# Kernel tuning notes

Measured on AMD Instinct MI355X. Metric: run time of the kernel, lower is better.

The kernel has to match this reference:

```python
import jax, jax.numpy as jnp
import numpy as np

B, S, D, H = 4, 2048, 768, 12
HD = D // H           # 64, also BigBird block size
BS, NB = 64, S // 64  # block size, num blocks
DFF = 4 * D
NEG = jnp.float32(-1e9)


def _bigbird_block_mask():
    # window(3) + global(first/last block rows+cols) + 3 random blocks per row
    rng = np.random.default_rng(0)
    m = np.zeros((NB, NB), dtype=bool)
    idx = np.arange(NB)
    for off in (-1, 0, 1):
        m[idx, np.clip(idx + off, 0, NB - 1)] = True
    m[0, :] = True; m[-1, :] = True; m[:, 0] = True; m[:, -1] = True
    rand_cols = rng.integers(0, NB, size=(NB, 3))
    m[idx[:, None], rand_cols] = True
    return m


def setup_inputs() -> dict:
    key = jax.random.key(0)
    ks = jax.random.split(key, 12)
    sc = 0.02
    inp = {
        "q": jax.random.normal(ks[0], (B, S, D), jnp.float32),
        "encoder_out": jax.random.normal(ks[1], (B, S, D), jnp.float32),
        "bb_mask": jnp.asarray(_bigbird_block_mask()),
        "Wq_s": jax.random.normal(ks[2], (D, D), jnp.float32) * sc,
        "Wk_s": jax.random.normal(ks[3], (D, D), jnp.float32) * sc,
        "Wv_s": jax.random.normal(ks[4], (D, D), jnp.float32) * sc,
        "Wo_s": jax.random.normal(ks[5], (D, D), jnp.float32) * sc,
        "Wq_c": jax.random.normal(ks[6], (D, D), jnp.float32) * sc,
        "Wk_c": jax.random.normal(ks[7], (D, D), jnp.float32) * sc,
        "Wv_c": jax.random.normal(ks[8], (D, D), jnp.float32) * sc,
        "Wo_c": jax.random.normal(ks[9], (D, D), jnp.float32) * sc,
        "ln_g": jnp.ones((D,), jnp.float32),
        "ln_b": jnp.zeros((D,), jnp.float32),
        "W1": jax.random.normal(ks[10], (D, DFF), jnp.float32) * sc,
        "b1": jnp.zeros((DFF,), jnp.float32),
        "W2": jax.random.normal(ks[11], (DFF, D), jnp.float32) * sc,
        "b2": jnp.zeros((D,), jnp.float32),
    }
    return inp


def _ln(x, g, b):
    mu = jnp.mean(x, -1, keepdims=True)
    var = jnp.mean(jnp.square(x - mu), -1, keepdims=True)
    return (x - mu) * jax.lax.rsqrt(var + 1e-5) * g + b


def _mha(xq, xkv, Wq, Wk, Wv, Wo, mask):
    # mask: [Sq, Sk] bool, True = attend
    b, sq, _ = xq.shape
    sk = xkv.shape[1]
    q = (xq @ Wq).reshape(b, sq, H, HD).transpose(0, 2, 1, 3)
    k = (xkv @ Wk).reshape(b, sk, H, HD).transpose(0, 2, 1, 3)
    v = (xkv @ Wv).reshape(b, sk, H, HD).transpose(0, 2, 1, 3)
    scores = jnp.einsum('bhqd,bhkd->bhqk', q, k) / jnp.sqrt(jnp.float32(HD))
    scores = jnp.where(mask[None, None], scores, NEG)
    attn = jax.nn.softmax(scores, axis=-1)
    o = jnp.einsum('bhqk,bhkd->bhqd', attn, v).transpose(0, 2, 1, 3).reshape(b, sq, D)
    return o @ Wo


def reference(q, encoder_out, bb_mask,
              Wq_s, Wk_s, Wv_s, Wo_s,
              Wq_c, Wk_c, Wv_c, Wo_c,
              ln_g, ln_b, W1, b1, W2, b2):
    # expand block mask to element level [S, S]
    el = jnp.repeat(jnp.repeat(bb_mask, BS, axis=0), BS, axis=1)
    causal = jnp.tril(jnp.ones((S, S), bool))
    m_self = el & causal
    x = q + _mha(_ln(q, ln_g, ln_b), _ln(q, ln_g, ln_b), Wq_s, Wk_s, Wv_s, Wo_s, m_self)
    x = x + _mha(_ln(x, ln_g, ln_b), encoder_out, Wq_c, Wk_c, Wv_c, Wo_c, el)
    h = _ln(x, ln_g, ln_b)
    x = x + (jax.nn.relu(h @ W1 + b1) @ W2 + b2)
    return x
```

## Files before the change

### kernel.cpp

```cpp
#include <hip/hip_runtime.h>
#include <hip/hip_bf16.h>

#define S_LEN 2048
#define DIM   768
#define NHEAD 12
#define HDIM  64
#define NBLK  32
#define BTOK  8192
#define DFF_  3072

typedef __attribute__((ext_vector_type(8))) short bf16x8;
typedef __attribute__((ext_vector_type(4))) float f32x4;

__device__ __forceinline__ void glds16(const void* g, void* l) {
  __builtin_amdgcn_global_load_lds(
      (const __attribute__((address_space(1))) void*)g,
      (__attribute__((address_space(3))) void*)l, 16, 0, 0);
}

__device__ __forceinline__ unsigned short bfbits(float f) {
  __hip_bfloat16 t = __float2bfloat16(f);
  return *(unsigned short*)&t;
}

__global__ void mask_norm_k(const unsigned char* __restrict__ p,
                            unsigned char* __restrict__ out) {
  int i = blockIdx.x * 256 + threadIdx.x;
  if (i < NBLK * NBLK) {
    bool byteLayout = (p[1] != 0);
    out[i] = byteLayout ? (unsigned char)(p[i] != 0)
                        : (unsigned char)(((const int*)p)[i] != 0);
  }
}

__device__ __forceinline__ float blockReduceSum256(float v) {
  v += __shfl_down(v, 32); v += __shfl_down(v, 16); v += __shfl_down(v, 8);
  v += __shfl_down(v, 4);  v += __shfl_down(v, 2);  v += __shfl_down(v, 1);
  __shared__ float sm[4];
  int w = threadIdx.x >> 6;
  __syncthreads();
  if ((threadIdx.x & 63) == 0) sm[w] = v;
  __syncthreads();
  return sm[0] + sm[1] + sm[2] + sm[3];
}

__global__ __launch_bounds__(256) void ln_k(const float* __restrict__ x,
                                            const float* __restrict__ g,
                                            const float* __restrict__ b,
                                            __hip_bfloat16* __restrict__ y) {
  size_t row = blockIdx.x;
  const float* xr = x + row * DIM;
  int t = threadIdx.x;
  float v0 = xr[t], v1 = xr[t + 256], v2 = xr[t + 512];
  float tot = blockReduceSum256(v0 + v1 + v2);
  float mu = tot * (1.0f / DIM);
  float d0 = v0 - mu, d1 = v1 - mu, d2 = v2 - mu;
  float var = blockReduceSum256(d0 * d0 + d1 * d1 + d2 * d2) * (1.0f / DIM);
  float rstd = rsqrtf(var + 1e-5f);
  __hip_bfloat16* yr = y + row * DIM;
  yr[t]       = __float2bfloat16(d0 * rstd * g[t]       + b[t]);
  yr[t + 256] = __float2bfloat16(d1 * rstd * g[t + 256] + b[t + 256]);
  yr[t + 512] = __float2bfloat16(d2 * rstd * g[t + 512] + b[t + 512]);
}

__global__ __launch_bounds__(256) void castbf_k(const float* __restrict__ x,
                                                __hip_bfloat16* __restrict__ y,
                                                int n) {
  int i = (blockIdx.x * 256 + threadIdx.x) * 8;
  if (i < n) {
    float4 v0 = *(const float4*)(x + i);
    float4 v1 = *(const float4*)(x + i + 4);
    union { bf16x8 v; unsigned short u[8]; } pk;
    pk.u[0] = bfbits(v0.x); pk.u[1] = bfbits(v0.y);
    pk.u[2] = bfbits(v0.z); pk.u[3] = bfbits(v0.w);
    pk.u[4] = bfbits(v1.x); pk.u[5] = bfbits(v1.y);
    pk.u[6] = bfbits(v1.z); pk.u[7] = bfbits(v1.w);
    *(bf16x8*)((unsigned short*)y + i) = pk.v;
  }
}

__global__ __launch_bounds__(256) void tcast_k(const float* __restrict__ W,
                                               __hip_bfloat16* __restrict__ Wt,
                                               int R, int C) {
  __shared__ float T[64][65];
  int r0 = blockIdx.y * 64, c0 = blockIdx.x * 64;
  int t = threadIdx.x;
  int r = t >> 2, cg = (t & 3) * 16;
  #pragma unroll
  for (int ii = 0; ii < 16; ii += 4) {
    float4 v = *(const float4*)(W + (size_t)(r0 + r) * C + c0 + cg + ii);
    T[r][cg + ii + 0] = v.x; T[r][cg + ii + 1] = v.y;
    T[r][cg + ii + 2] = v.z; T[r][cg + ii + 3] = v.w;
  }
  __syncthreads();
  int oc = t >> 2, og = (t & 3) * 16;
  union { bf16x8 v; unsigned short u[8]; } p0, p1;
  #pragma unroll
  for (int ii = 0; ii < 8; ++ii) p0.u[ii] = bfbits(T[og + ii][oc]);
  #pragma unroll
  for (int ii = 0; ii < 8; ++ii) p1.u[ii] = bfbits(T[og + 8 + ii][oc]);
  unsigned short* dst = (unsigned short*)Wt + (size_t)(c0 + oc) * R + r0 + og;
  *(bf16x8*)dst = p0.v;
  *(bf16x8*)(dst + 8) = p1.v;
}

template<bool BF16OUT, bool HASBIAS, bool HASRES, bool RELU, bool TRANSV>
__global__ __launch_bounds__(256) void mgemm_k(
    const __hip_bfloat16* __restrict__ A,
    const __hip_bfloat16* __restrict__ Bt,
    const float* __restrict__ bias,
    const float* __restrict__ resid,
    void* __restrict__ Cout,
    int M, int N, int K) {
  __shared__ char Asl[128 * 128];
  __shared__ char Bsl[128 * 128];
  int tid = threadIdx.x, w = tid >> 6, lane = tid & 63;
  int g = lane >> 4, cc = lane & 15;
  int wr = w >> 1, wc = w & 1;
  int m0 = blockIdx.y * 128, n0 = blockIdx.x * 128;

  f32x4 acc[4][4];
  #pragma unroll
  for (int i = 0; i < 4; ++i)
    #pragma unroll
    for (int j = 0; j < 4; ++j) acc[i][j] = (f32x4){0.f, 0.f, 0.f, 0.f};

  for (int k0 = 0; k0 < K; k0 += 64) {
    __syncthreads();
    #pragma unroll
    for (int ii = 0; ii < 4; ++ii) {
      int chunk = ii * 256 + w * 64 + lane;
      int row = chunk >> 3, hh = chunk & 7;
      int koff = k0 + ((hh ^ (row & 7)) << 3);
      glds16(A  + (size_t)(m0 + row) * K + koff, Asl + (ii * 256 + w * 64) * 16);
      glds16(Bt + (size_t)(n0 + row) * K + koff, Bsl + (ii * 256 + w * 64) * 16);
    }
    __syncthreads();
    bf16x8 a[4][2], b[4][2];
    #pragma unroll
    for (int i = 0; i < 4; ++i)
      #pragma unroll
      for (int s = 0; s < 2; ++s) {
        int row = wr * 64 + i * 16 + cc;
        a[i][s] = *(const bf16x8*)(Asl + row * 128 + (((s * 4 + g) ^ (cc & 7)) << 4));
      }
    #pragma unroll
    for (int j = 0; j < 4; ++j)
      #pragma unroll
      for (int s = 0; s < 2; ++s) {
        int row = wc * 64 + j * 16 + cc;
        b[j][s] = *(const bf16x8*)(Bsl + row * 128 + (((s * 4 + g) ^ (cc & 7)) << 4));
      }
    #pragma unroll
    for (int i = 0; i < 4; ++i)
      #pragma unroll
      for (int j = 0; j < 4; ++j)
        #pragma unroll
        for (int s = 0; s < 2; ++s)
          acc[i][j] = __builtin_amdgcn_mfma_f32_16x16x32_bf16(a[i][s], b[j][s], acc[i][j], 0, 0, 0);
  }
  #pragma unroll
  for (int i = 0; i < 4; ++i)
    #pragma unroll
    for (int j = 0; j < 4; ++j)
      #pragma unroll
      for (int e = 0; e < 4; ++e) {
        int r   = m0 + wr * 64 + i * 16 + g * 4 + e;
        int col = n0 + wc * 64 + j * 16 + cc;
        float v = acc[i][j][e];
        if (HASBIAS) v += bias[col];
        if (HASRES)  v += resid[(size_t)r * N + col];
        if (RELU)    v = fmaxf(v, 0.f);
        if (TRANSV) {
          int bb = r >> 11, s = r & 2047;
          ((__hip_bfloat16*)Cout)[(size_t)bb * DIM * S_LEN + (size_t)col * S_LEN + s] = __float2bfloat16(v);
        } else if (BF16OUT) {
          ((__hip_bfloat16*)Cout)[(size_t)r * N + col] = __float2bfloat16(v);
        } else {
          ((float*)Cout)[(size_t)r * N + col] = v;
        }
      }
}

template<bool CAUSAL>
__global__ __launch_bounds__(64) void mattn_k(
    const __hip_bfloat16* __restrict__ Qg,
    const __hip_bfloat16* __restrict__ Kg,
    const __hip_bfloat16* __restrict__ Vtg,
    __hip_bfloat16* __restrict__ O,
    const unsigned char* __restrict__ mask) {
  __shared__ char Ps[2048];
  int strip = blockIdx.x, h = blockIdx.y, b = blockIdx.z;
  int qb = strip >> 2, wq = strip & 3;
  int lane = threadIdx.x;
  int g = lane >> 4, cc = lane & 15;
  const unsigned short* Qp = (const unsigned short*)Qg;
  const unsigned short* Kp = (const unsigned short*)Kg;
  const unsigned short* Vp = (const unsigned short*)Vtg;

  bf16x8 aq[2];
  size_t qrow = ((size_t)b * S_LEN + strip * 16 + cc) * DIM + h * HDIM;
  aq[0] = *(const bf16x8*)(Qp + qrow + g * 8);
  aq[1] = *(const bf16x8*)(Qp + qrow + (4 + g) * 8);

  float m_[4], l_[4];
  f32x4 accO[4];
  #pragma unroll
  for (int e = 0; e < 4; ++e) { m_[e] = -3.0e38f; l_[e] = 0.f; }
  #pragma unroll
  for (int j = 0; j < 4; ++j) accO[j] = (f32x4){0.f, 0.f, 0.f, 0.f};

  int kbEnd = CAUSAL ? (qb + 1) : NBLK;
  for (int kb = 0; kb < kbEnd; ++kb) {
    if (!mask[qb * NBLK + kb]) continue;

    f32x4 S[4];
    #pragma unroll
    for (int j = 0; j < 4; ++j) S[j] = (f32x4){0.f, 0.f, 0.f, 0.f};
    #pragma unroll
    for (int j = 0; j < 4; ++j) {
      size_t krow = ((size_t)b * S_LEN + kb * 64 + j * 16 + cc) * DIM + h * HDIM;
      bf16x8 bk0 = *(const bf16x8*)(Kp + krow + g * 8);
      bf16x8 bk1 = *(const bf16x8*)(Kp + krow + (4 + g) * 8);
      S[j] = __builtin_amdgcn_mfma_f32_16x16x32_bf16(aq[0], bk0, S[j], 0, 0, 0);
      S[j] = __builtin_amdgcn_mfma_f32_16x16x32_bf16(aq[1], bk1, S[j], 0, 0, 0);
    }

    float p_[4][4];
    #pragma unroll
    for (int e = 0; e < 4; ++e) {
      float mm = -3.0e38f;
      #pragma unroll
      for (int j = 0; j < 4; ++j) {
        float sv = S[j][e] * 0.125f;
        if (CAUSAL && kb == qb) {
          int ql = wq * 16 + g * 4 + e, kl = j * 16 + cc;
          if (kl > ql) sv = -1e9f;
        }
        p_[j][e] = sv;
        mm = fmaxf(mm, sv);
      }
      mm = fmaxf(mm, __shfl_xor(mm, 1));
      mm = fmaxf(mm, __shfl_xor(mm, 2));
      mm = fmaxf(mm, __shfl_xor(mm, 4));
      mm = fmaxf(mm, __shfl_xor(mm, 8));
      float newm = fmaxf(m_[e], mm);
      float corr = __expf(m_[e] - newm);
      float rs = 0.f;
      #pragma unroll
      for (int j = 0; j < 4; ++j) {
        float p = __expf(p_[j][e] - newm);
        p_[j][e] = p;
        rs += p;
      }
      rs += __shfl_xor(rs, 1); rs += __shfl_xor(rs, 2);
      rs += __shfl_xor(rs, 4); rs += __shfl_xor(rs, 8);
      l_[e] = l_[e] * corr + rs;
      m_[e] = newm;
      #pragma unroll
      for (int j = 0; j < 4; ++j) accO[j][e] *= corr;
      int ql = g * 4 + e;
      #pragma unroll
      for (int j = 0; j < 4; ++j) {
        int kv = j * 16 + cc;
        int byt = ql * 128 + ((((kv >> 3) ^ (ql & 7))) << 4) + ((kv & 7) << 1);
        *(unsigned short*)(Ps + byt) = bfbits(p_[j][e]);
      }
    }

    #pragma unroll
    for (int s = 0; s < 2; ++s) {
      bf16x8 ap = *(const bf16x8*)(Ps + cc * 128 + (((s * 4 + g) ^ (cc & 7)) << 4));
      #pragma unroll
      for (int j = 0; j < 4; ++j) {
        size_t vrow = ((size_t)b * DIM + h * HDIM + j * 16 + cc) * S_LEN + kb * 64;
        bf16x8 bv = *(const bf16x8*)(Vp + vrow + (s * 4 + g) * 8);
        accO[j] = __builtin_amdgcn_mfma_f32_16x16x32_bf16(ap, bv, accO[j], 0, 0, 0);
      }
    }
  }
  #pragma unroll
  for (int e = 0; e < 4; ++e) {
    float inv = 1.0f / fmaxf(l_[e], 1e-30f);
    int tok = b * S_LEN + strip * 16 + g * 4 + e;
    #pragma unroll
    for (int j = 0; j < 4; ++j)
      O[(size_t)tok * DIM + h * HDIM + j * 16 + cc] = __float2bfloat16(accO[j][e] * inv);
  }
}

extern "C" void kernel_launch(void* const* d_in, const int* in_sizes, int n_in,
                              void* d_out, int out_size, void* d_ws, size_t ws_size,
                              hipStream_t stream) {
  const float* q    = (const float*)d_in[0];
  const float* enc  = (const float*)d_in[1];
  const unsigned char* bbm = (const unsigned char*)d_in[2];
  const float* Wsrc[8] = {(const float*)d_in[3], (const float*)d_in[4],
                          (const float*)d_in[5], (const float*)d_in[6],
                          (const float*)d_in[7], (const float*)d_in[8],
                          (const float*)d_in[9], (const float*)d_in[10]};
  const float* ln_g = (const float*)d_in[11];
  const float* ln_b = (const float*)d_in[12];
  const float* W1   = (const float*)d_in[13];
  const float* b1   = (const float*)d_in[14];
  const float* W2   = (const float*)d_in[15];
  const float* b2   = (const float*)d_in[16];

  char* ws = (char*)d_ws;
  unsigned char* maskn = (unsigned char*)ws;
  const size_t WT1 = (size_t)DIM * DIM * 2;
  __hip_bfloat16* Wt[8];
  for (int i = 0; i < 8; ++i) Wt[i] = (__hip_bfloat16*)(ws + 4096 + i * WT1);
  __hip_bfloat16* W1t  = (__hip_bfloat16*)(ws + 9441280);
  __hip_bfloat16* W2t  = (__hip_bfloat16*)(ws + 14159872);
  __hip_bfloat16* Ebf  = (__hip_bfloat16*)(ws + 18878464);
  float*          X    = (float*)         (ws + 31461376);
  __hip_bfloat16* Abf  = (__hip_bfloat16*)(ws + 56627200);
  __hip_bfloat16* Bq   = (__hip_bfloat16*)(ws + 69210112);
  __hip_bfloat16* Bk   = (__hip_bfloat16*)(ws + 81793024);
  __hip_bfloat16* Vt   = (__hip_bfloat16*)(ws + 94375936);
  __hip_bfloat16* Cc   = (__hip_bfloat16*)(ws + 106958848);
  __hip_bfloat16* F    = Bq;

  dim3 blk(256);
  dim3 gsq(12, 12), gw1(48, 12), gw2(12, 48);
  dim3 g768(6, 64), gff(24, 64);
  dim3 ga(128, NHEAD, 4);
  dim3 wv(64);

  mask_norm_k<<<4, blk, 0, stream>>>(bbm, maskn);
  for (int i = 0; i < 8; ++i)
    tcast_k<<<gsq, blk, 0, stream>>>(Wsrc[i], Wt[i], DIM, DIM);
  tcast_k<<<gw1, blk, 0, stream>>>(W1, W1t, DIM, DFF_);
  tcast_k<<<gw2, blk, 0, stream>>>(W2, W2t, DFF_, DIM);
  castbf_k<<<3072, blk, 0, stream>>>(enc, Ebf, BTOK * DIM);

  ln_k<<<BTOK, blk, 0, stream>>>(q, ln_g, ln_b, Abf);
  mgemm_k<true,false,false,false,false><<<g768, blk, 0, stream>>>(Abf, Wt[0], nullptr, nullptr, Bq, BTOK, DIM, DIM);
  mgemm_k<true,false,false,false,false><<<g768, blk, 0, stream>>>(Abf, Wt[1], nullptr, nullptr, Bk, BTOK, DIM, DIM);
  mgemm_k<true,false,false,false,true ><<<g768, blk, 0, stream>>>(Abf, Wt[2], nullptr, nullptr, Vt, BTOK, DIM, DIM);
  mattn_k<true><<<ga, wv, 0, stream>>>(Bq, Bk, Vt, Cc, maskn);
  mgemm_k<false,false,true,false,false><<<g768, blk, 0, stream>>>(Cc, Wt[3], nullptr, q, X, BTOK, DIM, DIM);

  ln_k<<<BTOK, blk, 0, stream>>>(X, ln_g, ln_b, Abf);
  mgemm_k<true,false,false,false,false><<<g768, blk, 0, stream>>>(Abf, Wt[4], nullptr, nullptr, Bq, BTOK, DIM, DIM);
  mgemm_k<true,false,false,false,false><<<g768, blk, 0, stream>>>(Ebf, Wt[5], nullptr, nullptr, Bk, BTOK, DIM, DIM);
  mgemm_k<true,false,false,false,true ><<<g768, blk, 0, stream>>>(Ebf, Wt[6], nullptr, nullptr, Vt, BTOK, DIM, DIM);
  mattn_k<false><<<ga, wv, 0, stream>>>(Bq, Bk, Vt, Cc, maskn);
  mgemm_k<false,false,true,false,false><<<g768, blk, 0, stream>>>(Cc, Wt[7], nullptr, X, X, BTOK, DIM, DIM);

  ln_k<<<BTOK, blk, 0, stream>>>(X, ln_g, ln_b, Abf);
  mgemm_k<true,true,false,true,false><<<gff, blk, 0, stream>>>(Abf, W1t, b1, nullptr, F, BTOK, DFF_, DIM);
  mgemm_k<false,true,true,false,false><<<g768, blk, 0, stream>>>(F, W2t, b2, X, d_out, BTOK, DIM, DFF_);

  (void)in_sizes; (void)n_in; (void)out_size; (void)ws_size;
}
```

Before: 895.8 us.

## Group four attention waves per block, prefetch next K/V tile, remap grid

The sparse attention kernel now launches 256-thread blocks in which four waves cover the four 16-row strips of one query block, each with its own LDS slice for P. K and V fragments for the next active key block are loaded into registers while the current block is computed, so global load latency overlaps the MFMA and softmax work. The 1D grid is remapped with an 8-way interleave over (batch, head, query-block) slots to spread work across dispatch. This adds register pressure from the double-buffered K/V fragments, which may lower occupancy. The causal kernel also gives blocks uneven work.

```diff
diff --git a/kernel.cpp b/kernel.cpp
--- a/kernel.cpp
+++ b/kernel.cpp
@@ -182,26 +182,47 @@
       }
 }
 
+#define LOADK(kbv, dst)                                                       \
+  { _Pragma("unroll")                                                         \
+    for (int j = 0; j < 4; ++j) {                                             \
+      size_t kro = ((size_t)b * S_LEN + (kbv) * 64 + j * 16 + cc) * DIM       \
+                   + h * HDIM + g * 8;                                        \
+      dst[j][0] = *(const bf16x8*)(Kp + kro);                                 \
+      dst[j][1] = *(const bf16x8*)(Kp + kro + 32);                            \
+    } }
+#define LOADV(kbv, dst)                                                       \
+  { _Pragma("unroll")                                                         \
+    for (int j = 0; j < 4; ++j) {                                             \
+      size_t vro = ((size_t)b * DIM + h * HDIM + j * 16 + cc) * S_LEN         \
+                   + (kbv) * 64 + g * 8;                                      \
+      dst[j][0] = *(const bf16x8*)(Vp + vro);                                 \
+      dst[j][1] = *(const bf16x8*)(Vp + vro + 32);                            \
+    } }
+
 template<bool CAUSAL>
-__global__ __launch_bounds__(64) void mattn_k(
+__global__ __launch_bounds__(256) void mattn_k(
     const __hip_bfloat16* __restrict__ Qg,
     const __hip_bfloat16* __restrict__ Kg,
     const __hip_bfloat16* __restrict__ Vtg,
     __hip_bfloat16* __restrict__ O,
     const unsigned char* __restrict__ mask) {
-  __shared__ char Ps[2048];
-  int strip = blockIdx.x, h = blockIdx.y, b = blockIdx.z;
-  int qb = strip >> 2, wq = strip & 3;
-  int lane = threadIdx.x;
+  __shared__ char Ps[8192];
+  int lin = blockIdx.x;
+  int slot = (lin & 7) * 192 + (lin >> 3);
+  int pair = slot >> 5, qb = slot & 31;
+  int h = pair % NHEAD, b = pair / NHEAD;
+  int t = threadIdx.x, w = t >> 6, lane = t & 63;
   int g = lane >> 4, cc = lane & 15;
+  int strip = qb * 4 + w;
+  char* Pw = Ps + w * 2048;
   const unsigned short* Qp = (const unsigned short*)Qg;
   const unsigned short* Kp = (const unsigned short*)Kg;
   const unsigned short* Vp = (const unsigned short*)Vtg;
 
-  bf16x8 aq[2];
+  bf16x8 aq0, aq1;
   size_t qrow = ((size_t)b * S_LEN + strip * 16 + cc) * DIM + h * HDIM;
-  aq[0] = *(const bf16x8*)(Qp + qrow + g * 8);
-  aq[1] = *(const bf16x8*)(Qp + qrow + (4 + g) * 8);
+  aq0 = *(const bf16x8*)(Qp + qrow + g * 8);
+  aq1 = *(const bf16x8*)(Qp + qrow + (4 + g) * 8);
 
   float m_[4], l_[4];
   f32x4 accO[4];
@@ -210,20 +231,27 @@
   #pragma unroll
   for (int j = 0; j < 4; ++j) accO[j] = (f32x4){0.f, 0.f, 0.f, 0.f};
 
+  const unsigned char* mrow = mask + qb * NBLK;
   int kbEnd = CAUSAL ? (qb + 1) : NBLK;
-  for (int kb = 0; kb < kbEnd; ++kb) {
-    if (!mask[qb * NBLK + kb]) continue;
+
+  int cur = 0;
+  while (!mrow[cur]) ++cur;
+  bf16x8 kc[4][2], vc[4][2];
+  LOADK(cur, kc); LOADV(cur, vc);
+
+  for (;;) {
+    int nxt = cur + 1;
+    while (nxt < kbEnd && !mrow[nxt]) ++nxt;
+    bool more = (nxt < kbEnd);
+    bf16x8 kn[4][2], vn[4][2];
+    if (more) { LOADK(nxt, kn); LOADV(nxt, vn); }
 
     f32x4 S[4];
     #pragma unroll
-    for (int j = 0; j < 4; ++j) S[j] = (f32x4){0.f, 0.f, 0.f, 0.f};
-    #pragma unroll
     for (int j = 0; j < 4; ++j) {
-      size_t krow = ((size_t)b * S_LEN + kb * 64 + j * 16 + cc) * DIM + h * HDIM;
-      bf16x8 bk0 = *(const bf16x8*)(Kp + krow + g * 8);
-      bf16x8 bk1 = *(const bf16x8*)(Kp + krow + (4 + g) * 8);
-      S[j] = __builtin_amdgcn_mfma_f32_16x16x32_bf16(aq[0], bk0, S[j], 0, 0, 0);
-      S[j] = __builtin_amdgcn_mfma_f32_16x16x32_bf16(aq[1], bk1, S[j], 0, 0, 0);
+      S[j] = (f32x4){0.f, 0.f, 0.f, 0.f};
+      S[j] = __builtin_amdgcn_mfma_f32_16x16x32_bf16(aq0, kc[j][0], S[j], 0, 0, 0);
+      S[j] = __builtin_amdgcn_mfma_f32_16x16x32_bf16(aq1, kc[j][1], S[j], 0, 0, 0);
     }
 
     float p_[4][4];
@@ -233,8 +261,8 @@
       #pragma unroll
       for (int j = 0; j < 4; ++j) {
         float sv = S[j][e] * 0.125f;
-        if (CAUSAL && kb == qb) {
-          int ql = wq * 16 + g * 4 + e, kl = j * 16 + cc;
+        if (CAUSAL && cur == qb) {
+          int ql = w * 16 + g * 4 + e, kl = j * 16 + cc;
           if (kl > ql) sv = -1e9f;
         }
         p_[j][e] = sv;
@@ -264,21 +292,27 @@
       for (int j = 0; j < 4; ++j) {
         int kv = j * 16 + cc;
         int byt = ql * 128 + ((((kv >> 3) ^ (ql & 7))) << 4) + ((kv & 7) << 1);
-        *(unsigned short*)(Ps + byt) = bfbits(p_[j][e]);
+        *(unsigned short*)(Pw + byt) = bfbits(p_[j][e]);
       }
     }
 
     #pragma unroll
     for (int s = 0; s < 2; ++s) {
-      bf16x8 ap = *(const bf16x8*)(Ps + cc * 128 + (((s * 4 + g) ^ (cc & 7)) << 4));
-      #pragma unroll
-      for (int j = 0; j < 4; ++j) {
-        size_t vrow = ((size_t)b * DIM + h * HDIM + j * 16 + cc) * S_LEN + kb * 64;
-        bf16x8 bv = *(const bf16x8*)(Vp + vrow + (s * 4 + g) * 8);
-        accO[j] = __builtin_amdgcn_mfma_f32_16x16x32_bf16(ap, bv, accO[j], 0, 0, 0);
-      }
-    }
-  }
+      bf16x8 ap = *(const bf16x8*)(Pw + cc * 128 + (((s * 4 + g) ^ (cc & 7)) << 4));
+      #pragma unroll
+      for (int j = 0; j < 4; ++j)
+        accO[j] = __builtin_amdgcn_mfma_f32_16x16x32_bf16(ap, vc[j][s], accO[j], 0, 0, 0);
+    }
+
+    if (!more) break;
+    #pragma unroll
+    for (int j = 0; j < 4; ++j) {
+      kc[j][0] = kn[j][0]; kc[j][1] = kn[j][1];
+      vc[j][0] = vn[j][0]; vc[j][1] = vn[j][1];
+    }
+    cur = nxt;
+  }
+
   #pragma unroll
   for (int e = 0; e < 4; ++e) {
     float inv = 1.0f / fmaxf(l_[e], 1e-30f);
@@ -325,8 +359,7 @@
   dim3 blk(256);
   dim3 gsq(12, 12), gw1(48, 12), gw2(12, 48);
   dim3 g768(6, 64), gff(24, 64);
-  dim3 ga(128, NHEAD, 4);
-  dim3 wv(64);
+  dim3 ga(1536);
 
   mask_norm_k<<<4, blk, 0, stream>>>(bbm, maskn);
   for (int i = 0; i < 8; ++i)
@@ -339,14 +372,14 @@
   mgemm_k<true,false,false,false,false><<<g768, blk, 0, stream>>>(Abf, Wt[0], nullptr, nullptr, Bq, BTOK, DIM, DIM);
   mgemm_k<true,false,false,false,false><<<g768, blk, 0, stream>>>(Abf, Wt[1], nullptr, nullptr, Bk, BTOK, DIM, DIM);
   mgemm_k<true,false,false,false,true ><<<g768, blk, 0, stream>>>(Abf, Wt[2], nullptr, nullptr, Vt, BTOK, DIM, DIM);
-  mattn_k<true><<<ga, wv, 0, stream>>>(Bq, Bk, Vt, Cc, maskn);
+  mattn_k<true><<<ga, blk, 0, stream>>>(Bq, Bk, Vt, Cc, maskn);
   mgemm_k<false,false,true,false,false><<<g768, blk, 0, stream>>>(Cc, Wt[3], nullptr, q, X, BTOK, DIM, DIM);
 
   ln_k<<<BTOK, blk, 0, stream>>>(X, ln_g, ln_b, Abf);
   mgemm_k<true,false,false,false,false><<<g768, blk, 0, stream>>>(Abf, Wt[4], nullptr, nullptr, Bq, BTOK, DIM, DIM);
   mgemm_k<true,false,false,false,false><<<g768, blk, 0, stream>>>(Ebf, Wt[5], nullptr, nullptr, Bk, BTOK, DIM, DIM);
   mgemm_k<true,false,false,false,true ><<<g768, blk, 0, stream>>>(Ebf, Wt[6], nullptr, nullptr, Vt, BTOK, DIM, DIM);
-  mattn_k<false><<<ga, wv, 0, stream>>>(Bq, Bk, Vt, Cc, maskn);
+  mattn_k<false><<<ga, blk, 0, stream>>>(Bq, Bk, Vt, Cc, maskn);
   mgemm_k<false,false,true,false,false><<<g768, blk, 0, stream>>>(Cc, Wt[7], nullptr, X, X, BTOK, DIM, DIM);
 
   ln_k<<<BTOK, blk, 0, stream>>>(X, ln_g, ln_b, Abf);
```

After: 864.8 us. 1.04x faster.

## Fuse QKV projections and restructure sparse attention with lazy rescaling and balanced scheduling

Applied to the files above, without the earlier changes.

The self-attention Q/K/V projections become one GEMM with N=2304 over the contiguous transposed weights, and the cross-attention K/V projections become one GEMM with N=1536. The epilogue routes each 768-column range to its own buffer, writing V transposed. The attention kernel now computes S transposed (K as the A operand), so softmax needs fewer cross-lane reductions. It prefetches K and V fragments into registers, rescales the running max lazily only when it grows by more than 8, packs P stores into 64-bit writes, and remaps the flat grid so causal-heavy query blocks are spread across XCDs. The aims are fewer launches, fewer re-reads of the A activations, less softmax shuffle and exp overhead, and better load balance. The cost is more register pressure and per-element branching in the GEMM epilogue.

```diff
diff --git a/kernel.cpp b/kernel.cpp
--- a/kernel.cpp
+++ b/kernel.cpp
@@ -18,9 +18,9 @@
       (__attribute__((address_space(3))) void*)l, 16, 0, 0);
 }
 
-__device__ __forceinline__ unsigned short bfbits(float f) {
+__device__ __forceinline__ unsigned int bfbits(float f) {
   __hip_bfloat16 t = __float2bfloat16(f);
-  return *(unsigned short*)&t;
+  return (unsigned int)*(unsigned short*)&t;
 }
 
 __global__ void mask_norm_k(const unsigned char* __restrict__ p,
@@ -104,13 +104,13 @@
   *(bf16x8*)(dst + 8) = p1.v;
 }
 
-template<bool BF16OUT, bool HASBIAS, bool HASRES, bool RELU, bool TRANSV>
+template<bool BF16OUT, bool HASBIAS, bool HASRES, bool RELU, int SPLIT>
 __global__ __launch_bounds__(256) void mgemm_k(
     const __hip_bfloat16* __restrict__ A,
     const __hip_bfloat16* __restrict__ Bt,
     const float* __restrict__ bias,
     const float* __restrict__ resid,
-    void* __restrict__ Cout,
+    void* __restrict__ o1, void* __restrict__ o2, void* __restrict__ o3,
     int M, int N, int K) {
   __shared__ char Asl[128 * 128];
   __shared__ char Bsl[128 * 128];
@@ -159,6 +159,7 @@
         for (int s = 0; s < 2; ++s)
           acc[i][j] = __builtin_amdgcn_mfma_f32_16x16x32_bf16(a[i][s], b[j][s], acc[i][j], 0, 0, 0);
   }
+  int range = n0 / 768;
   #pragma unroll
   for (int i = 0; i < 4; ++i)
     #pragma unroll
@@ -171,13 +172,20 @@
         if (HASBIAS) v += bias[col];
         if (HASRES)  v += resid[(size_t)r * N + col];
         if (RELU)    v = fmaxf(v, 0.f);
-        if (TRANSV) {
-          int bb = r >> 11, s = r & 2047;
-          ((__hip_bfloat16*)Cout)[(size_t)bb * DIM * S_LEN + (size_t)col * S_LEN + s] = __float2bfloat16(v);
-        } else if (BF16OUT) {
-          ((__hip_bfloat16*)Cout)[(size_t)r * N + col] = __float2bfloat16(v);
+        if (SPLIT == 0) {
+          if (BF16OUT) ((__hip_bfloat16*)o1)[(size_t)r * N + col] = __float2bfloat16(v);
+          else         ((float*)o1)[(size_t)r * N + col] = v;
         } else {
-          ((float*)Cout)[(size_t)r * N + col] = v;
+          int cl = col - range * 768;
+          void* dst; bool trans;
+          if (SPLIT == 1) { dst = range == 0 ? o1 : (range == 1 ? o2 : o3); trans = (range == 2); }
+          else            { dst = range == 0 ? o1 : o2;                      trans = (range == 1); }
+          if (trans) {
+            int bb = r >> 11, s = r & 2047;
+            ((__hip_bfloat16*)dst)[(size_t)bb * DIM * S_LEN + (size_t)cl * S_LEN + s] = __float2bfloat16(v);
+          } else {
+            ((__hip_bfloat16*)dst)[(size_t)r * 768 + cl] = __float2bfloat16(v);
+          }
         }
       }
 }
@@ -190,98 +198,123 @@
     __hip_bfloat16* __restrict__ O,
     const unsigned char* __restrict__ mask) {
   __shared__ char Ps[2048];
-  int strip = blockIdx.x, h = blockIdx.y, b = blockIdx.z;
-  int qb = strip >> 2, wq = strip & 3;
+  int lin = blockIdx.x;
+  int slot = (lin & 7) * 768 + (lin >> 3);
+  int pair = slot >> 7, sl = slot & 127;
+  int rawqb = sl >> 2, w = sl & 3;
+  int qb = CAUSAL ? (31 - rawqb)
+                  : ((rawqb & 1) ? (31 - (rawqb >> 1)) : (rawqb >> 1));
+  int h = pair % NHEAD, b = pair / NHEAD;
   int lane = threadIdx.x;
   int g = lane >> 4, cc = lane & 15;
+  int strip = qb * 4 + w;
   const unsigned short* Qp = (const unsigned short*)Qg;
   const unsigned short* Kp = (const unsigned short*)Kg;
   const unsigned short* Vp = (const unsigned short*)Vtg;
 
-  bf16x8 aq[2];
+  bf16x8 aq0, aq1;
   size_t qrow = ((size_t)b * S_LEN + strip * 16 + cc) * DIM + h * HDIM;
-  aq[0] = *(const bf16x8*)(Qp + qrow + g * 8);
-  aq[1] = *(const bf16x8*)(Qp + qrow + (4 + g) * 8);
-
-  float m_[4], l_[4];
+  aq0 = *(const bf16x8*)(Qp + qrow + g * 8);
+  aq1 = *(const bf16x8*)(Qp + qrow + (4 + g) * 8);
+
+  float m_ = -1e30f, l_ = 0.f;
   f32x4 accO[4];
   #pragma unroll
-  for (int e = 0; e < 4; ++e) { m_[e] = -3.0e38f; l_[e] = 0.f; }
-  #pragma unroll
   for (int j = 0; j < 4; ++j) accO[j] = (f32x4){0.f, 0.f, 0.f, 0.f};
 
+  const unsigned char* mrow = mask + qb * NBLK;
   int kbEnd = CAUSAL ? (qb + 1) : NBLK;
+
   for (int kb = 0; kb < kbEnd; ++kb) {
-    if (!mask[qb * NBLK + kb]) continue;
+    if (!mrow[kb]) continue;
+
+    bf16x8 kc[4][2], vc[4][2];
+    #pragma unroll
+    for (int j = 0; j < 4; ++j) {
+      size_t kro = ((size_t)b * S_LEN + kb * 64 + j * 16 + cc) * DIM + h * HDIM + g * 8;
+      kc[j][0] = *(const bf16x8*)(Kp + kro);
+      kc[j][1] = *(const bf16x8*)(Kp + kro + 32);
+      size_t vro = ((size_t)b * DIM + h * HDIM + j * 16 + cc) * S_LEN + kb * 64 + g * 8;
+      vc[j][0] = *(const bf16x8*)(Vp + vro);
+      vc[j][1] = *(const bf16x8*)(Vp + vro + 32);
+    }
 
     f32x4 S[4];
     #pragma unroll
-    for (int j = 0; j < 4; ++j) S[j] = (f32x4){0.f, 0.f, 0.f, 0.f};
-    #pragma unroll
     for (int j = 0; j < 4; ++j) {
-      size_t krow = ((size_t)b * S_LEN + kb * 64 + j * 16 + cc) * DIM + h * HDIM;
-      bf16x8 bk0 = *(const bf16x8*)(Kp + krow + g * 8);
-      bf16x8 bk1 = *(const bf16x8*)(Kp + krow + (4 + g) * 8);
-      S[j] = __builtin_amdgcn_mfma_f32_16x16x32_bf16(aq[0], bk0, S[j], 0, 0, 0);
-      S[j] = __builtin_amdgcn_mfma_f32_16x16x32_bf16(aq[1], bk1, S[j], 0, 0, 0);
-    }
-
-    float p_[4][4];
-    #pragma unroll
-    for (int e = 0; e < 4; ++e) {
-      float mm = -3.0e38f;
-      #pragma unroll
-      for (int j = 0; j < 4; ++j) {
+      S[j] = (f32x4){0.f, 0.f, 0.f, 0.f};
+      S[j] = __builtin_amdgcn_mfma_f32_16x16x32_bf16(kc[j][0], aq0, S[j], 0, 0, 0);
+      S[j] = __builtin_amdgcn_mfma_f32_16x16x32_bf16(kc[j][1], aq1, S[j], 0, 0, 0);
+    }
+
+    float p[4][4];
+    float mmL = -1e30f;
+    #pragma unroll
+    for (int j = 0; j < 4; ++j)
+      #pragma unroll
+      for (int e = 0; e < 4; ++e) {
         float sv = S[j][e] * 0.125f;
         if (CAUSAL && kb == qb) {
-          int ql = wq * 16 + g * 4 + e, kl = j * 16 + cc;
-          if (kl > ql) sv = -1e9f;
+          int kwi = j * 16 + g * 4 + e, qwi = w * 16 + cc;
+          if (kwi > qwi) sv = -1e9f;
         }
-        p_[j][e] = sv;
-        mm = fmaxf(mm, sv);
-      }
-      mm = fmaxf(mm, __shfl_xor(mm, 1));
-      mm = fmaxf(mm, __shfl_xor(mm, 2));
-      mm = fmaxf(mm, __shfl_xor(mm, 4));
-      mm = fmaxf(mm, __shfl_xor(mm, 8));
-      float newm = fmaxf(m_[e], mm);
-      float corr = __expf(m_[e] - newm);
-      float rs = 0.f;
-      #pragma unroll
-      for (int j = 0; j < 4; ++j) {
-        float p = __expf(p_[j][e] - newm);
-        p_[j][e] = p;
-        rs += p;
-      }
-      rs += __shfl_xor(rs, 1); rs += __shfl_xor(rs, 2);
-      rs += __shfl_xor(rs, 4); rs += __shfl_xor(rs, 8);
-      l_[e] = l_[e] * corr + rs;
-      m_[e] = newm;
-      #pragma unroll
-      for (int j = 0; j < 4; ++j) accO[j][e] *= corr;
-      int ql = g * 4 + e;
-      #pragma unroll
-      for (int j = 0; j < 4; ++j) {
-        int kv = j * 16 + cc;
-        int byt = ql * 128 + ((((kv >> 3) ^ (ql & 7))) << 4) + ((kv & 7) << 1);
-        *(unsigned short*)(Ps + byt) = bfbits(p_[j][e]);
-      }
+        p[j][e] = sv;
+        mmL = fmaxf(mmL, sv);
+      }
+
+    if (!__all(mmL <= m_ + 8.0f)) {
+      float mm = fmaxf(mmL, __shfl_xor(mmL, 16));
+      mm = fmaxf(mm, __shfl_xor(mm, 32));
+      float newm = fmaxf(m_, mm);
+      float corr = __expf(m_ - newm);
+      m_ = newm;
+      l_ *= corr;
+      #pragma unroll
+      for (int e = 0; e < 4; ++e) {
+        int src = (lane & 48) | (g * 4 + e);
+        float ce = __shfl(corr, src);
+        #pragma unroll
+        for (int j = 0; j < 4; ++j) accO[j][e] *= ce;
+      }
+    }
+
+    float rs = 0.f;
+    #pragma unroll
+    for (int j = 0; j < 4; ++j)
+      #pragma unroll
+      for (int e = 0; e < 4; ++e) {
+        float pe = __expf(p[j][e] - m_);
+        p[j][e] = pe;
+        rs += pe;
+      }
+    l_ += rs;
+
+    #pragma unroll
+    for (int j = 0; j < 4; ++j) {
+      unsigned int lo = bfbits(p[j][0]) | (bfbits(p[j][1]) << 16);
+      unsigned int hi = bfbits(p[j][2]) | (bfbits(p[j][3]) << 16);
+      int kv0 = j * 16 + g * 4;
+      int byt = cc * 128 + (((kv0 >> 3) ^ (cc & 7)) << 4) + ((kv0 & 7) << 1);
+      *(unsigned long long*)(Ps + byt) =
+          (unsigned long long)lo | ((unsigned long long)hi << 32);
     }
 
     #pragma unroll
     for (int s = 0; s < 2; ++s) {
       bf16x8 ap = *(const bf16x8*)(Ps + cc * 128 + (((s * 4 + g) ^ (cc & 7)) << 4));
       #pragma unroll
-      for (int j = 0; j < 4; ++j) {
-        size_t vrow = ((size_t)b * DIM + h * HDIM + j * 16 + cc) * S_LEN + kb * 64;
-        bf16x8 bv = *(const bf16x8*)(Vp + vrow + (s * 4 + g) * 8);
-        accO[j] = __builtin_amdgcn_mfma_f32_16x16x32_bf16(ap, bv, accO[j], 0, 0, 0);
-      }
-    }
-  }
+      for (int j = 0; j < 4; ++j)
+        accO[j] = __builtin_amdgcn_mfma_f32_16x16x32_bf16(ap, vc[j][s], accO[j], 0, 0, 0);
+    }
+  }
+
+  float lt = l_ + __shfl_xor(l_, 16);
+  lt += __shfl_xor(lt, 32);
   #pragma unroll
   for (int e = 0; e < 4; ++e) {
-    float inv = 1.0f / fmaxf(l_[e], 1e-30f);
+    int src = (lane & 48) | (g * 4 + e);
+    float le = __shfl(lt, src);
+    float inv = 1.0f / fmaxf(le, 1e-30f);
     int tok = b * S_LEN + strip * 16 + g * 4 + e;
     #pragma unroll
     for (int j = 0; j < 4; ++j)
@@ -324,8 +357,8 @@
 
   dim3 blk(256);
   dim3 gsq(12, 12), gw1(48, 12), gw2(12, 48);
-  dim3 g768(6, 64), gff(24, 64);
-  dim3 ga(128, NHEAD, 4);
+  dim3 g768(6, 64), gqkv(18, 64), gkv(12, 64), gff(24, 64);
+  dim3 ga(6144);
   dim3 wv(64);
 
   mask_norm_k<<<4, blk, 0, stream>>>(bbm, maskn);
@@ -336,22 +369,26 @@
   castbf_k<<<3072, blk, 0, stream>>>(enc, Ebf, BTOK * DIM);
 
   ln_k<<<BTOK, blk, 0, stream>>>(q, ln_g, ln_b, Abf);
-  mgemm_k<true,false,false,false,false><<<g768, blk, 0, stream>>>(Abf, Wt[0], nullptr, nullptr, Bq, BTOK, DIM, DIM);
-  mgemm_k<true,false,false,false,false><<<g768, blk, 0, stream>>>(Abf, Wt[1], nullptr, nullptr, Bk, BTOK, DIM, DIM);
-  mgemm_k<true,false,false,false,true ><<<g768, blk, 0, stream>>>(Abf, Wt[2], nullptr, nullptr, Vt, BTOK, DIM, DIM);
+  mgemm_k<true,false,false,false,1><<<gqkv, blk, 0, stream>>>(
+      Abf, Wt[0], nullptr, nullptr, Bq, Bk, Vt, BTOK, 2304, DIM);
   mattn_k<true><<<ga, wv, 0, stream>>>(Bq, Bk, Vt, Cc, maskn);
-  mgemm_k<false,false,true,false,false><<<g768, blk, 0, stream>>>(Cc, Wt[3], nullptr, q, X, BTOK, DIM, DIM);
+  mgemm_k<false,false,true,false,0><<<g768, blk, 0, stream>>>(
+      Cc, Wt[3], nullptr, q, X, nullptr, nullptr, BTOK, DIM, DIM);
 
   ln_k<<<BTOK, blk, 0, stream>>>(X, ln_g, ln_b, Abf);
-  mgemm_k<true,false,false,false,false><<<g768, blk, 0, stream>>>(Abf, Wt[4], nullptr, nullptr, Bq, BTOK, DIM, DIM);
-  mgemm_k<true,false,false,false,false><<<g768, blk, 0, stream>>>(Ebf, Wt[5], nullptr, nullptr, Bk, BTOK, DIM, DIM);
-  mgemm_k<true,false,false,false,true ><<<g768, blk, 0, stream>>>(Ebf, Wt[6], nullptr, nullptr, Vt, BTOK, DIM, DIM);
+  mgemm_k<true,false,false,false,0><<<g768, blk, 0, stream>>>(
+      Abf, Wt[4], nullptr, nullptr, Bq, nullptr, nullptr, BTOK, DIM, DIM);
+  mgemm_k<true,false,false,false,2><<<gkv, blk, 0, stream>>>(
+      Ebf, Wt[5], nullptr, nullptr, Bk, Vt, nullptr, BTOK, 1536, DIM);
   mattn_k<false><<<ga, wv, 0, stream>>>(Bq, Bk, Vt, Cc, maskn);
-  mgemm_k<false,false,true,false,false><<<g768, blk, 0, stream>>>(Cc, Wt[7], nullptr, X, X, BTOK, DIM, DIM);
+  mgemm_k<false,false,true,false,0><<<g768, blk, 0, stream>>>(
+      Cc, Wt[7], nullptr, X, X, nullptr, nullptr, BTOK, DIM, DIM);
 
   ln_k<<<BTOK, blk, 0, stream>>>(X, ln_g, ln_b, Abf);
-  mgemm_k<true,true,false,true,false><<<gff, blk, 0, stream>>>(Abf, W1t, b1, nullptr, F, BTOK, DFF_, DIM);
-  mgemm_k<false,true,true,false,false><<<g768, blk, 0, stream>>>(F, W2t, b2, X, d_out, BTOK, DIM, DFF_);
+  mgemm_k<true,true,false,true,0><<<gff, blk, 0, stream>>>(
+      Abf, W1t, b1, nullptr, F, nullptr, nullptr, BTOK, DFF_, DIM);
+  mgemm_k<false,true,true,false,0><<<g768, blk, 0, stream>>>(
+      F, W2t, b2, X, d_out, nullptr, nullptr, BTOK, DIM, DFF_);
 
   (void)in_sizes; (void)n_in; (void)out_size; (void)ws_size;
 }
```

Measured after the change: 729.0 us. 18.6% less time.
